# Kernel tuning notes

Hardware: AMD Instinct MI355X
Metric: run time of the kernel (lower is better)

The kernel has to match this reference:

```python
import jax, jax.numpy as jnp
import numpy as np

B, S, D, K = 2048, 200, 64, 4  # batch, seq_len, dim, num_interest


def setup_inputs() -> dict:
    key = jax.random.key(0)
    k1, k2, k3, k4 = jax.random.split(key, 4)
    item_his_emb = jax.random.normal(k1, (B, S, D), dtype=jnp.float32)
    item_eb = jax.random.normal(k2, (B, D), dtype=jnp.float32)
    mask = jax.random.randint(k3, (B, S), 0, 2, dtype=jnp.int32)
    W = jax.random.normal(k4, (D, K * D), dtype=jnp.float32) * 0.05
    b = jnp.zeros((K * D,), dtype=jnp.float32)
    return {"item_his_emb": item_his_emb, "item_eb": item_eb, "mask": mask, "W": W, "b": b}


def _squash(v):
    # v: [B, K, D]; squash nonlinearity with the module's epsilon
    n2 = jnp.sum(jnp.square(v), axis=-1, keepdims=True)
    return (n2 / (1.0 + n2) / jnp.sqrt(n2 + 1e-9)) * v


def reference(item_his_emb, item_eb, mask, W, b):
    # bilinear_type == 1: Dense(dim * num_interest)
    hat = item_his_emb @ W + b                      # [B, S, K*D]
    hat = hat.reshape(B, S, K, D).transpose(0, 2, 1, 3)  # [B, K, S, D]

    mask_zero = (mask == 0)[:, None, :]             # [B, 1, S] broadcast over K
    cw = jnp.zeros((B, K, S), dtype=item_his_emb.dtype)

    interest = None
    for i in range(3):
        sw = jax.nn.softmax(cw, axis=1)             # softmax over interests
        sw = jnp.where(mask_zero, 0.0, sw)          # [B, K, S]
        interest = _squash(jnp.einsum('bks,bksd->bkd', sw, hat))  # [B, K, D]
        if i < 2:
            cw = cw + jnp.einsum('bksd,bkd->bks', hat, interest)

    # readout: softmax attention over interests against target item, hard argmax gather
    atten = jax.nn.softmax(jnp.einsum('bkd,bd->bk', interest, item_eb), axis=1)
    idx = jnp.argmax(atten, axis=1)                 # [B]
    readout = jnp.take_along_axis(interest, idx[:, None, None], axis=1)[:, 0, :]  # [B, D]
    return interest, readout
```

## Files before the change

### kernel.cpp

```cpp
#include <hip/hip_runtime.h>


#define NB 2048
#define NS 200
#define ND 64
#define NK 4
#define NT 512

__device__ __forceinline__ float wred64(float v) {
#pragma unroll
  for (int o = 1; o < 64; o <<= 1) v += __shfl_xor(v, o, 64);
  return v;
}

__device__ __forceinline__ int rot(int s) { return (s + (s >> 3)) & 15; }

__device__ __forceinline__ void gload16(const float* g_, float* l_) {
  __builtin_amdgcn_global_load_lds(
      (const __attribute__((address_space(1))) unsigned int*)g_,
      (__attribute__((address_space(3))) unsigned int*)l_, 16, 0, 0);
}

#define RED_GRP(v) v += __shfl_xor(v, 16, 64); v += __shfl_xor(v, 32, 64);

__global__ __launch_bounds__(NT, 4) void caps_kernel(
    const float* __restrict__ his, const float* __restrict__ itemeb,
    const int* __restrict__ mask, const float* __restrict__ W,
    const float* __restrict__ bias, float* __restrict__ out) {
  __shared__ float semb[NS * ND];
  __shared__ float ssw[NS * NK];
  __shared__ float pe[8][NK][ND];
  __shared__ float sG[NK][ND];
  __shared__ float su[NK][ND];
  __shared__ float pts[8][NK];
  __shared__ float soff[NK], satt[NK];
  __shared__ int sidx;

  const int t = threadIdx.x;
  const int w = t >> 6, l = t & 63;
  const int g = l >> 4, j = l & 15;
  const int gid = (w << 2) | g;
  const int ke = w & 3, h_ = w >> 2;
  const int b = blockIdx.x;
  const float* eb = his + (size_t)b * NS * ND;

  float wreg[32];
#pragma unroll
  for (int c = 0; c < 32; ++c)
    wreg[c] = W[(size_t)(32 * h_ + c) * (NK * ND) + ke * ND + l];
  float breg = bias[ke * ND + l];
  float iq = itemeb[(size_t)b * ND + l];

  for (int i = w; i < 50; i += 8) {
    int s = 4 * i + g;
    int q = (j - rot(s)) & 15;
    gload16(eb + (s << 6) + (q << 2), &semb[i * 256]);
  }
  if (t < NS) {
    float m = (mask[(size_t)b * NS + t] != 0) ? 0.25f : 0.0f;
    *(float4*)&ssw[t * 4] = make_float4(m, m, m, m);
  }
  __syncthreads();

  for (int it = 0; it < 3; ++it) {
    if (it > 0) {
      const int row = t >> 1, p = t & 1;
      if (row < NS) {
        const int rr = rot(row);
        float lg0 = 0.f, lg1 = 0.f, lg2 = 0.f, lg3 = 0.f;
#pragma unroll
        for (int cc = 0; cc < 8; ++cc) {
          int jj = 8 * p + cc;
          float4 eq = *(const float4*)&semb[(row << 6) + 4 * ((jj + rr) & 15)];
          float4 u0 = *(const float4*)&su[0][4 * jj];
          float4 u1 = *(const float4*)&su[1][4 * jj];
          float4 u2 = *(const float4*)&su[2][4 * jj];
          float4 u3 = *(const float4*)&su[3][4 * jj];
          lg0 += eq.x * u0.x + eq.y * u0.y + eq.z * u0.z + eq.w * u0.w;
          lg1 += eq.x * u1.x + eq.y * u1.y + eq.z * u1.z + eq.w * u1.w;
          lg2 += eq.x * u2.x + eq.y * u2.y + eq.z * u2.z + eq.w * u2.w;
          lg3 += eq.x * u3.x + eq.y * u3.y + eq.z * u3.z + eq.w * u3.w;
        }
        lg0 += __shfl_xor(lg0, 1, 64);
        lg1 += __shfl_xor(lg1, 1, 64);
        lg2 += __shfl_xor(lg2, 1, 64);
        lg3 += __shfl_xor(lg3, 1, 64);
        lg0 += soff[0]; lg1 += soff[1]; lg2 += soff[2]; lg3 += soff[3];
        float mx = fmaxf(fmaxf(lg0, lg1), fmaxf(lg2, lg3));
        float e0 = __expf(lg0 - mx), e1 = __expf(lg1 - mx);
        float e2 = __expf(lg2 - mx), e3 = __expf(lg3 - mx);
        float mv = (mask[(size_t)b * NS + row] != 0) ? 1.0f : 0.0f;
        float r = mv / (e0 + e1 + e2 + e3);
        if (p == 0)
          *(float4*)&ssw[row * 4] = make_float4(e0 * r, e1 * r, e2 * r, e3 * r);
      }
      __syncthreads();
    }

    float4 a0 = {0, 0, 0, 0}, a1 = {0, 0, 0, 0}, a2 = {0, 0, 0, 0},
           a3 = {0, 0, 0, 0};
    float t0 = 0, t1 = 0, t2 = 0, t3 = 0;
    const int ntr = (w < 2) ? 7 : 6;
    for (int tt = 0; tt < ntr; ++tt) {
      int s = gid + 32 * tt;
      float4 eq = *(const float4*)&semb[(s << 6) + 4 * ((j + rot(s)) & 15)];
      float4 s4 = *(const float4*)&ssw[s * 4];
      a0.x += s4.x * eq.x; a0.y += s4.x * eq.y; a0.z += s4.x * eq.z; a0.w += s4.x * eq.w;
      a1.x += s4.y * eq.x; a1.y += s4.y * eq.y; a1.z += s4.y * eq.z; a1.w += s4.y * eq.w;
      a2.x += s4.z * eq.x; a2.y += s4.z * eq.y; a2.z += s4.z * eq.z; a2.w += s4.z * eq.w;
      a3.x += s4.w * eq.x; a3.y += s4.w * eq.y; a3.z += s4.w * eq.z; a3.w += s4.w * eq.w;
      t0 += s4.x; t1 += s4.y; t2 += s4.z; t3 += s4.w;
    }
    RED_GRP(a0.x) RED_GRP(a0.y) RED_GRP(a0.z) RED_GRP(a0.w)
    RED_GRP(a1.x) RED_GRP(a1.y) RED_GRP(a1.z) RED_GRP(a1.w)
    RED_GRP(a2.x) RED_GRP(a2.y) RED_GRP(a2.z) RED_GRP(a2.w)
    RED_GRP(a3.x) RED_GRP(a3.y) RED_GRP(a3.z) RED_GRP(a3.w)
    RED_GRP(t0) RED_GRP(t1) RED_GRP(t2) RED_GRP(t3)
    if (l < 16) {
      *(float4*)&pe[w][0][4 * l] = a0;
      *(float4*)&pe[w][1][4 * l] = a1;
      *(float4*)&pe[w][2][4 * l] = a2;
      *(float4*)&pe[w][3][4 * l] = a3;
    }
    if (l == 0) { pts[w][0] = t0; pts[w][1] = t1; pts[w][2] = t2; pts[w][3] = t3; }
    __syncthreads();

    {
      int cl = 32 * h_ + (l & 31);
      float sse = 0.f;
#pragma unroll
      for (int w2 = 0; w2 < 8; ++w2) sse += pe[w2][ke][cl];
      su[ke][cl] = sse;
      float vp = 0.f;
#pragma unroll
      for (int q2 = 0; q2 < 8; ++q2) {
        float4 e4 = *(const float4*)&su[ke][32 * h_ + 4 * q2];
        vp += e4.x * wreg[4 * q2 + 0] + e4.y * wreg[4 * q2 + 1] +
              e4.z * wreg[4 * q2 + 2] + e4.w * wreg[4 * q2 + 3];
      }
      if (h_) ssw[ke * 64 + l] = vp;
      __syncthreads();

      if (h_ == 0) {
        float ts_ = 0.f;
#pragma unroll
        for (int w2 = 0; w2 < 8; ++w2) ts_ += pts[w2][ke];
        float accv = vp + ssw[ke * 64 + l] + ts_ * breg;
        float n2 = wred64(accv * accv);
        float scale = n2 / (1.f + n2) / sqrtf(n2 + 1e-9f);
        float inter = scale * accv;
        if (it < 2) {
          float gnew = (it == 0) ? inter : (sG[ke][l] + inter);
          sG[ke][l] = gnew;
          float ob = wred64(breg * gnew);
          if (l == 0) soff[ke] = ob;
          const float4* Wr =
              (const float4*)(W + (size_t)l * (NK * ND) + ke * ND);
          const float4* Gk = (const float4*)&sG[ke][0];
          float a = 0.f;
#pragma unroll
          for (int d4 = 0; d4 < 16; ++d4) {
            float4 wv = Wr[d4], gv = Gk[d4];
            a += wv.x * gv.x + wv.y * gv.y + wv.z * gv.z + wv.w * gv.w;
          }
          su[ke][l] = a;
        } else {
          out[((size_t)b * NK + ke) * ND + l] = inter;
          float dot_ = wred64(inter * iq);
          pe[0][ke][l] = inter;
          if (l == 0) satt[ke] = dot_;
        }
      }
      __syncthreads();
    }
  }

  if (t == 0) {
    int bi = 0;
    float bv = satt[0];
#pragma unroll
    for (int kk = 1; kk < NK; ++kk)
      if (satt[kk] > bv) { bv = satt[kk]; bi = kk; }
    sidx = bi;
  }
  __syncthreads();
  if (t < ND) out[(size_t)NB * NK * ND + (size_t)b * ND + t] = pe[0][sidx][t];
}

extern "C" void kernel_launch(void* const* d_in, const int* in_sizes, int n_in,
                              void* d_out, int out_size, void* d_ws, size_t ws_size,
                              hipStream_t stream) {
  (void)in_sizes; (void)n_in; (void)out_size; (void)d_ws; (void)ws_size;
  const float* his = (const float*)d_in[0];
  const float* itemeb = (const float*)d_in[1];
  const int* mask = (const int*)d_in[2];
  const float* W = (const float*)d_in[3];
  const float* bias = (const float*)d_in[4];
  float* out = (float*)d_out;
  caps_kernel<<<NB, NT, 0, stream>>>(his, itemeb, mask, W, bias, out);
}
```

Baseline: 92.23 us.

## Fuse routing-logit softmax into weighted-sum pass and drop ssw buffer

The separate per-row logit/softmax phase and its barrier are merged into the weighted accumulation loop. Each 16-lane group computes the four routing logits with shuffle reductions, applies softmax and the mask, and accumulates directly, so the shared ssw buffer is no longer needed. Iteration 0 computes a single uniform-weight sum and copies it to all four interests. Launch bounds drop from 4 to 2 blocks per SIMD, which allows more registers but may lower occupancy. The fused path adds 16 shuffles per row for the logit reductions.

```diff
diff --git a/kernel.cpp b/kernel.cpp
--- a/kernel.cpp
+++ b/kernel.cpp
@@ -22,18 +22,23 @@
 }
 
 #define RED_GRP(v) v += __shfl_xor(v, 16, 64); v += __shfl_xor(v, 32, 64);
-
-__global__ __launch_bounds__(NT, 4) void caps_kernel(
+#define RED_16(v)                                        \
+  v += __shfl_xor(v, 1, 64); v += __shfl_xor(v, 2, 64);  \
+  v += __shfl_xor(v, 4, 64); v += __shfl_xor(v, 8, 64);
+
+__global__ __launch_bounds__(NT, 2) void caps_kernel(
     const float* __restrict__ his, const float* __restrict__ itemeb,
     const int* __restrict__ mask, const float* __restrict__ W,
     const float* __restrict__ bias, float* __restrict__ out) {
   __shared__ float semb[NS * ND];
-  __shared__ float ssw[NS * NK];
   __shared__ float pe[8][NK][ND];
   __shared__ float sG[NK][ND];
   __shared__ float su[NK][ND];
+  __shared__ float spv[NK][ND];
+  __shared__ float smsk[NS];
   __shared__ float pts[8][NK];
-  __shared__ float soff[NK], satt[NK];
+  __shared__ __align__(16) float soff[NK];
+  __shared__ float satt[NK];
   __shared__ int sidx;
 
   const int t = threadIdx.x;
@@ -56,66 +61,60 @@
     int q = (j - rot(s)) & 15;
     gload16(eb + (s << 6) + (q << 2), &semb[i * 256]);
   }
-  if (t < NS) {
-    float m = (mask[(size_t)b * NS + t] != 0) ? 0.25f : 0.0f;
-    *(float4*)&ssw[t * 4] = make_float4(m, m, m, m);
-  }
+  if (t < NS) smsk[t] = (mask[(size_t)b * NS + t] != 0) ? 1.0f : 0.0f;
   __syncthreads();
 
+  const int ntr = (w < 2) ? 7 : 6;
+
   for (int it = 0; it < 3; ++it) {
-    if (it > 0) {
-      const int row = t >> 1, p = t & 1;
-      if (row < NS) {
-        const int rr = rot(row);
-        float lg0 = 0.f, lg1 = 0.f, lg2 = 0.f, lg3 = 0.f;
-#pragma unroll
-        for (int cc = 0; cc < 8; ++cc) {
-          int jj = 8 * p + cc;
-          float4 eq = *(const float4*)&semb[(row << 6) + 4 * ((jj + rr) & 15)];
-          float4 u0 = *(const float4*)&su[0][4 * jj];
-          float4 u1 = *(const float4*)&su[1][4 * jj];
-          float4 u2 = *(const float4*)&su[2][4 * jj];
-          float4 u3 = *(const float4*)&su[3][4 * jj];
-          lg0 += eq.x * u0.x + eq.y * u0.y + eq.z * u0.z + eq.w * u0.w;
-          lg1 += eq.x * u1.x + eq.y * u1.y + eq.z * u1.z + eq.w * u1.w;
-          lg2 += eq.x * u2.x + eq.y * u2.y + eq.z * u2.z + eq.w * u2.w;
-          lg3 += eq.x * u3.x + eq.y * u3.y + eq.z * u3.z + eq.w * u3.w;
-        }
-        lg0 += __shfl_xor(lg0, 1, 64);
-        lg1 += __shfl_xor(lg1, 1, 64);
-        lg2 += __shfl_xor(lg2, 1, 64);
-        lg3 += __shfl_xor(lg3, 1, 64);
-        lg0 += soff[0]; lg1 += soff[1]; lg2 += soff[2]; lg3 += soff[3];
+    float4 a0 = {0, 0, 0, 0}, a1 = {0, 0, 0, 0}, a2 = {0, 0, 0, 0},
+           a3 = {0, 0, 0, 0};
+    float t0 = 0, t1 = 0, t2 = 0, t3 = 0;
+
+    if (it == 0) {
+      for (int tt = 0; tt < ntr; ++tt) {
+        int s = gid + 32 * tt;
+        float4 eq = *(const float4*)&semb[(s << 6) + 4 * ((j + rot(s)) & 15)];
+        float sw = 0.25f * smsk[s];
+        a0.x += sw * eq.x; a0.y += sw * eq.y;
+        a0.z += sw * eq.z; a0.w += sw * eq.w;
+        t0 += sw;
+      }
+      RED_GRP(a0.x) RED_GRP(a0.y) RED_GRP(a0.z) RED_GRP(a0.w) RED_GRP(t0)
+      a1 = a0; a2 = a0; a3 = a0; t1 = t0; t2 = t0; t3 = t0;
+    } else {
+      float4 u0 = *(const float4*)&su[0][4 * j];
+      float4 u1 = *(const float4*)&su[1][4 * j];
+      float4 u2 = *(const float4*)&su[2][4 * j];
+      float4 u3 = *(const float4*)&su[3][4 * j];
+      float4 sof = *(const float4*)&soff[0];
+      for (int tt = 0; tt < ntr; ++tt) {
+        int s = gid + 32 * tt;
+        float4 eq = *(const float4*)&semb[(s << 6) + 4 * ((j + rot(s)) & 15)];
+        float mk = smsk[s];
+        float lg0 = eq.x * u0.x + eq.y * u0.y + eq.z * u0.z + eq.w * u0.w;
+        float lg1 = eq.x * u1.x + eq.y * u1.y + eq.z * u1.z + eq.w * u1.w;
+        float lg2 = eq.x * u2.x + eq.y * u2.y + eq.z * u2.z + eq.w * u2.w;
+        float lg3 = eq.x * u3.x + eq.y * u3.y + eq.z * u3.z + eq.w * u3.w;
+        RED_16(lg0) RED_16(lg1) RED_16(lg2) RED_16(lg3)
+        lg0 += sof.x; lg1 += sof.y; lg2 += sof.z; lg3 += sof.w;
         float mx = fmaxf(fmaxf(lg0, lg1), fmaxf(lg2, lg3));
         float e0 = __expf(lg0 - mx), e1 = __expf(lg1 - mx);
         float e2 = __expf(lg2 - mx), e3 = __expf(lg3 - mx);
-        float mv = (mask[(size_t)b * NS + row] != 0) ? 1.0f : 0.0f;
-        float r = mv / (e0 + e1 + e2 + e3);
-        if (p == 0)
-          *(float4*)&ssw[row * 4] = make_float4(e0 * r, e1 * r, e2 * r, e3 * r);
-      }
-      __syncthreads();
+        float r = mk / (e0 + e1 + e2 + e3);
+        float sw0 = e0 * r, sw1 = e1 * r, sw2 = e2 * r, sw3 = e3 * r;
+        a0.x += sw0 * eq.x; a0.y += sw0 * eq.y; a0.z += sw0 * eq.z; a0.w += sw0 * eq.w;
+        a1.x += sw1 * eq.x; a1.y += sw1 * eq.y; a1.z += sw1 * eq.z; a1.w += sw1 * eq.w;
+        a2.x += sw2 * eq.x; a2.y += sw2 * eq.y; a2.z += sw2 * eq.z; a2.w += sw2 * eq.w;
+        a3.x += sw3 * eq.x; a3.y += sw3 * eq.y; a3.z += sw3 * eq.z; a3.w += sw3 * eq.w;
+        t0 += sw0; t1 += sw1; t2 += sw2; t3 += sw3;
+      }
+      RED_GRP(a0.x) RED_GRP(a0.y) RED_GRP(a0.z) RED_GRP(a0.w)
+      RED_GRP(a1.x) RED_GRP(a1.y) RED_GRP(a1.z) RED_GRP(a1.w)
+      RED_GRP(a2.x) RED_GRP(a2.y) RED_GRP(a2.z) RED_GRP(a2.w)
+      RED_GRP(a3.x) RED_GRP(a3.y) RED_GRP(a3.z) RED_GRP(a3.w)
+      RED_GRP(t0) RED_GRP(t1) RED_GRP(t2) RED_GRP(t3)
     }
-
-    float4 a0 = {0, 0, 0, 0}, a1 = {0, 0, 0, 0}, a2 = {0, 0, 0, 0},
-           a3 = {0, 0, 0, 0};
-    float t0 = 0, t1 = 0, t2 = 0, t3 = 0;
-    const int ntr = (w < 2) ? 7 : 6;
-    for (int tt = 0; tt < ntr; ++tt) {
-      int s = gid + 32 * tt;
-      float4 eq = *(const float4*)&semb[(s << 6) + 4 * ((j + rot(s)) & 15)];
-      float4 s4 = *(const float4*)&ssw[s * 4];
-      a0.x += s4.x * eq.x; a0.y += s4.x * eq.y; a0.z += s4.x * eq.z; a0.w += s4.x * eq.w;
-      a1.x += s4.y * eq.x; a1.y += s4.y * eq.y; a1.z += s4.y * eq.z; a1.w += s4.y * eq.w;
-      a2.x += s4.z * eq.x; a2.y += s4.z * eq.y; a2.z += s4.z * eq.z; a2.w += s4.z * eq.w;
-      a3.x += s4.w * eq.x; a3.y += s4.w * eq.y; a3.z += s4.w * eq.z; a3.w += s4.w * eq.w;
-      t0 += s4.x; t1 += s4.y; t2 += s4.z; t3 += s4.w;
-    }
-    RED_GRP(a0.x) RED_GRP(a0.y) RED_GRP(a0.z) RED_GRP(a0.w)
-    RED_GRP(a1.x) RED_GRP(a1.y) RED_GRP(a1.z) RED_GRP(a1.w)
-    RED_GRP(a2.x) RED_GRP(a2.y) RED_GRP(a2.z) RED_GRP(a2.w)
-    RED_GRP(a3.x) RED_GRP(a3.y) RED_GRP(a3.z) RED_GRP(a3.w)
-    RED_GRP(t0) RED_GRP(t1) RED_GRP(t2) RED_GRP(t3)
     if (l < 16) {
       *(float4*)&pe[w][0][4 * l] = a0;
       *(float4*)&pe[w][1][4 * l] = a1;
@@ -138,14 +137,14 @@
         vp += e4.x * wreg[4 * q2 + 0] + e4.y * wreg[4 * q2 + 1] +
               e4.z * wreg[4 * q2 + 2] + e4.w * wreg[4 * q2 + 3];
       }
-      if (h_) ssw[ke * 64 + l] = vp;
+      if (h_) spv[ke][l] = vp;
       __syncthreads();
 
       if (h_ == 0) {
         float ts_ = 0.f;
 #pragma unroll
         for (int w2 = 0; w2 < 8; ++w2) ts_ += pts[w2][ke];
-        float accv = vp + ssw[ke * 64 + l] + ts_ * breg;
+        float accv = vp + spv[ke][l] + ts_ * breg;
         float n2 = wred64(accv * accv);
         float scale = n2 / (1.f + n2) / sqrtf(n2 + 1e-9f);
         float inter = scale * accv;
@@ -167,7 +166,7 @@
         } else {
           out[((size_t)b * NK + ke) * ND + l] = inter;
           float dot_ = wred64(inter * iq);
-          pe[0][ke][l] = inter;
+          spv[ke][l] = inter;
           if (l == 0) satt[ke] = dot_;
         }
       }
@@ -184,7 +183,7 @@
     sidx = bi;
   }
   __syncthreads();
-  if (t < ND) out[(size_t)NB * NK * ND + (size_t)b * ND + t] = pe[0][sidx][t];
+  if (t < ND) out[(size_t)NB * NK * ND + (size_t)b * ND + t] = spv[sidx][t];
 }
 
 extern "C" void kernel_launch(void* const* d_in, const int* in_sizes, int n_in,
```

Result: slower. 145.7 us (+58.0%).
